# Kernel optimization log

Measured on AMD Instinct MI355X. Metric: run time of the kernel, lower is better.

## Reference

```python
import jax, jax.numpy as jnp
import numpy as np

B, Q, K = 16, 100, 100
H, DM = 8, 512
DK = DM // H          # 64, per-head dim (= Attention embed_dim)
MID = 32              # mid_dim
EPS = 1e-5            # GroupNorm eps
NEG = -1000000000.0   # masked_fill value


def setup_inputs() -> dict:
    key = jax.random.key(0)
    ks = jax.random.split(key, 32)
    def n(k, shape, s=0.02):
        return jax.random.normal(k, shape, jnp.float32) * s
    inp = {
        "query": jax.random.normal(ks[0], (B, Q, DM), jnp.float32),
        "key":   jax.random.normal(ks[1], (B, K, DM), jnp.float32),
        "value": jax.random.normal(ks[2], (B, K, DM), jnp.float32),
        "mask":  jnp.ones((B, Q, K), jnp.float32),
        # 4 input projections: Linear(DM,DM) -> CELU -> GroupNorm(H, DM)
        "Wq1": n(ks[3], (DM, DM)), "bq1": jnp.zeros((DM,), jnp.float32),
        "gw1": jnp.ones((DM,), jnp.float32), "gb1": jnp.zeros((DM,), jnp.float32),
        "Wk":  n(ks[4], (DM, DM)), "bk":  jnp.zeros((DM,), jnp.float32),
        "gwk": jnp.ones((DM,), jnp.float32), "gbk": jnp.zeros((DM,), jnp.float32),
        "Wq2": n(ks[5], (DM, DM)), "bq2": jnp.zeros((DM,), jnp.float32),
        "gw2": jnp.ones((DM,), jnp.float32), "gb2": jnp.zeros((DM,), jnp.float32),
        "Wv":  n(ks[6], (DM, DM)), "bv":  jnp.zeros((DM,), jnp.float32),
        "gwv": jnp.ones((DM,), jnp.float32), "gbv": jnp.zeros((DM,), jnp.float32),
        # Attention MLPs (per-head, embed_dim = DK)
        "We":  n(ks[7], (MID, DK)), "be":  jnp.zeros((MID,), jnp.float32),
        "Ws":  n(ks[8], (1, MID)),  "bs":  jnp.zeros((1,), jnp.float32),
        "Wsq": n(ks[9], (DK, MID)), "bsq": jnp.zeros((DK,), jnp.float32),
    }
    return inp


def _proj(x, W, b, gw, gb):
    """Linear -> CELU -> GroupNorm(H groups over DM channels), then split heads.
    x: (B, L, DM) -> (B, H, L, DK)"""
    Bn, L, _ = x.shape
    y = jax.nn.celu(x.reshape(Bn * L, DM) @ W.T + b)
    yg = y.reshape(Bn * L, H, DK)
    mu = yg.mean(-1, keepdims=True)
    var = yg.var(-1, keepdims=True)
    yn = ((yg - mu) * jax.lax.rsqrt(var + EPS)).reshape(Bn * L, DM)
    yn = yn * gw + gb
    return yn.reshape(Bn, L, H, DK).transpose(0, 2, 1, 3)


def reference(query, key, value, mask,
              Wq1, bq1, gw1, gb1, Wk, bk, gwk, gbk,
              Wq2, bq2, gw2, gb2, Wv, bv, gwv, gbv,
              We, be, Ws, bs, Wsq, bsq):
    q1 = _proj(query, Wq1, bq1, gw1, gb1)   # (B,H,Q,DK)
    k  = _proj(key,   Wk,  bk,  gwk, gbk)   # (B,H,K,DK)
    q2 = _proj(query, Wq2, bq2, gw2, gb2)   # (B,H,Q,DK)
    v  = _proj(value, Wv,  bv,  gwv, gbv)   # (B,H,K,DK)

    m = mask[:, None]                        # (B,1,Q,K)
    # bilinear query-key map, embedded by Linear->ReLU (dropout=identity, eval)
    key_map = jnp.einsum('bhqd,bhkd->bhqkd', q1, k)          # (B,H,Q,K,DK)
    km = jax.nn.relu(jnp.einsum('bhqkd,md->bhqkm', key_map, We) + be)  # (B,H,Q,K,MID)

    alpha = jnp.einsum('bhqkm,m->bhqk', km, Ws[0]) + bs[0]   # (B,H,Q,K)
    alpha = jnp.where(m == 0, NEG, alpha)
    alpha = jax.nn.softmax(alpha, axis=-1)

    # masked mean pooling over K, then channel squeeze-excite
    pool = jnp.sum(km * m[..., None], axis=-2) / jnp.sum(m[..., None], axis=-2)  # (B,H,Q,MID)
    ch = jax.nn.sigmoid(pool @ Wsq.T + bsq)                  # (B,H,Q,DK)

    # spatial attention over val_map: sum_k alpha * (q2_d * v_kd) = q2 * (alpha @ v)
    sp = q2 * jnp.einsum('bhqk,bhkd->bhqd', alpha, v)        # (B,H,Q,DK)
    x = sp * ch
    return x.transpose(0, 2, 1, 3).reshape(x.shape[0], -1, DM)  # (B,Q,DM)
```

## Files before the change

kernel.cpp:

```cpp
#include <hip/hip_runtime.h>
#include <hip/hip_bf16.h>
#include <math.h>

#define H 8
#define DM 512
#define DK 64
#define MID 32
#define LL 100
#define EPS 1e-5f
#define NEGV -1000000000.0f

typedef unsigned short u16;
typedef __attribute__((ext_vector_type(8))) short short8b;
typedef __attribute__((ext_vector_type(16))) float f32x16;

#define MFMA32 __builtin_amdgcn_mfma_f32_32x32x16_bf16
#define GLD_LDS16(g, l) __builtin_amdgcn_global_load_lds( \
    (const __attribute__((address_space(1))) void*)(g), \
    (__attribute__((address_space(3))) void*)(l), 16, 0, 0)

__device__ __forceinline__ unsigned pkbf2(float a, float b) {
    union { __hip_bfloat162 h; unsigned u; } cv;
    cv.h = __float22bfloat162_rn(make_float2(a, b));
    return cv.u;
}
__device__ __forceinline__ u16 bfbits(float a) {
    union { __hip_bfloat16 b; u16 u; } cv;
    cv.b = __float2bfloat16(a);
    return cv.u;
}
__device__ __forceinline__ float bf2f(u16 u) {
    union { u16 u; __hip_bfloat16 b; } cv; cv.u = u;
    return __bfloat162float(cv.b);
}

__global__ __launch_bounds__(256) void cvt_kernel(
    const float* __restrict__ q, const float* __restrict__ k, const float* __restrict__ v,
    const float* __restrict__ w1, const float* __restrict__ wk,
    const float* __restrict__ w2, const float* __restrict__ wv,
    u16* __restrict__ qh, u16* __restrict__ qlo, u16* __restrict__ kh, u16* __restrict__ klo,
    u16* __restrict__ vh, u16* __restrict__ vlo,
    u16* __restrict__ w1h, u16* __restrict__ w1l, u16* __restrict__ wkh, u16* __restrict__ wkl,
    u16* __restrict__ w2h, u16* __restrict__ w2l, u16* __restrict__ wvh, u16* __restrict__ wvl)
{
    int f = blockIdx.x * 256 + threadIdx.x;
    const float* src; u16* dh; u16* dl; int off;
    if (f < 204800)      { src = q;  dh = qh;  dl = qlo; off = f; }
    else if (f < 409600) { src = k;  dh = kh;  dl = klo; off = f - 204800; }
    else if (f < 614400) { src = v;  dh = vh;  dl = vlo; off = f - 409600; }
    else if (f < 679936) { src = w1; dh = w1h; dl = w1l; off = f - 614400; }
    else if (f < 745472) { src = wk; dh = wkh; dl = wkl; off = f - 679936; }
    else if (f < 811008) { src = w2; dh = w2h; dl = w2l; off = f - 745472; }
    else                 { src = wv; dh = wvh; dl = wvl; off = f - 811008; }
    float4 x = *(const float4*)(src + (size_t)off * 4);
    u16 h0 = bfbits(x.x), h1 = bfbits(x.y), h2 = bfbits(x.z), h3 = bfbits(x.w);
    ushort4 hv; hv.x = h0; hv.y = h1; hv.z = h2; hv.w = h3;
    ushort4 lv;
    lv.x = bfbits(x.x - bf2f(h0)); lv.y = bfbits(x.y - bf2f(h1));
    lv.z = bfbits(x.z - bf2f(h2)); lv.w = bfbits(x.w - bf2f(h3));
    *(ushort4*)(dh + (size_t)off * 4) = hv;
    *(ushort4*)(dl + (size_t)off * 4) = lv;
}

__global__ __launch_bounds__(256) void proj_kernel(
    const u16* __restrict__ qh, const u16* __restrict__ qlo,
    const u16* __restrict__ kh, const u16* __restrict__ klo,
    const u16* __restrict__ vh, const u16* __restrict__ vlo,
    const u16* __restrict__ w1h, const u16* __restrict__ w1l,
    const u16* __restrict__ wkh, const u16* __restrict__ wkl,
    const u16* __restrict__ w2h, const u16* __restrict__ w2l,
    const u16* __restrict__ wvh, const u16* __restrict__ wvl,
    const float* __restrict__ bq1, const float* __restrict__ gw1, const float* __restrict__ gb1,
    const float* __restrict__ bk , const float* __restrict__ gwk, const float* __restrict__ gbk,
    const float* __restrict__ bq2, const float* __restrict__ gw2, const float* __restrict__ gb2,
    const float* __restrict__ bv , const float* __restrict__ gwv, const float* __restrict__ gbv,
    float* __restrict__ q1o, u16* __restrict__ kbf,
    float* __restrict__ q2o, u16* __restrict__ vtbf)
{
    __shared__ u16 sm[20480];
    __shared__ float lds_s[4][32];
    __shared__ float lds_q[4][32];
    u16* Xh = sm;          u16* Xl = sm + 2048;
    u16* Wh = sm + 4096;   u16* Wl = sm + 12288;

    const int rt = blockIdx.x;
    const int ct = blockIdx.y;
    const int p  = blockIdx.z;
    const int j0 = ct * 128;
    const int r0 = rt * 32;
    const int t = threadIdx.x, w = t >> 6, lane = t & 63, ql = lane & 31, hf = lane >> 5;

    const u16 *Xhg, *Xlg, *Whg, *Wlg; const float *bias, *gw, *gb;
    if (p == 0)      { Xhg=qh; Xlg=qlo; Whg=w1h; Wlg=w1l; bias=bq1; gw=gw1; gb=gb1; }
    else if (p == 1) { Xhg=kh; Xlg=klo; Whg=wkh; Wlg=wkl; bias=bk;  gw=gwk; gb=gbk; }
    else if (p == 2) { Xhg=qh; Xlg=qlo; Whg=w2h; Wlg=w2l; bias=bq2; gw=gw2; gb=gb2; }
    else             { Xhg=vh; Xlg=vlo; Whg=wvh; Wlg=wvl; bias=bv;  gw=gwv; gb=gbv; }

    f32x16 acc = {0.f,0.f,0.f,0.f,0.f,0.f,0.f,0.f,0.f,0.f,0.f,0.f,0.f,0.f,0.f,0.f};

    for (int kc = 0; kc < 8; ++kc) {
        __syncthreads();
        for (int i = w; i < 40; i += 4) {
            const u16* g; u16* l; int blk, rbase;
            if (i < 4)       { g = Xhg; l = Xh; blk = i;      rbase = r0; }
            else if (i < 8)  { g = Xlg; l = Xl; blk = i - 4;  rbase = r0; }
            else if (i < 24) { g = Whg; l = Wh; blk = i - 8;  rbase = j0; }
            else             { g = Wlg; l = Wl; blk = i - 24; rbase = j0; }
            int row = blk * 8 + (lane >> 3);
            int k16 = (lane & 7) ^ (row & 7);
            const u16* ga = g + (size_t)(rbase + row) * 512 + kc * 64 + k16 * 8;
            GLD_LDS16(ga, (char*)l + blk * 1024);
        }
        __syncthreads();
        const int brow = w * 32 + ql;
        #pragma unroll
        for (int ks = 0; ks < 4; ++ks) {
            int slot = (ks * 2 + hf) ^ (ql & 7);
            short8b Ah = *(const short8b*)(Xh + ql * 64 + slot * 8);
            short8b Al = *(const short8b*)(Xl + ql * 64 + slot * 8);
            short8b Bh = *(const short8b*)(Wh + brow * 64 + slot * 8);
            short8b Bl = *(const short8b*)(Wl + brow * 64 + slot * 8);
            acc = MFMA32(Ah, Bh, acc, 0, 0, 0);
            acc = MFMA32(Ah, Bl, acc, 0, 0, 0);
            acc = MFMA32(Al, Bh, acc, 0, 0, 0);
        }
    }

    const int colg = j0 + w * 32 + ql;
    const float bv_ = bias[colg];
    const float gwc = gw[colg], gbc = gb[colg];
    float y[16], s[16], sq[16];
    #pragma unroll
    for (int r = 0; r < 16; ++r) {
        float x = acc[r] + bv_;
        x = x > 0.f ? x : expm1f(x);
        y[r] = x; s[r] = x; sq[r] = x * x;
    }
    #pragma unroll
    for (int off = 1; off < 32; off <<= 1) {
        #pragma unroll
        for (int r = 0; r < 16; ++r) {
            s[r]  += __shfl_xor(s[r],  off, 64);
            sq[r] += __shfl_xor(sq[r], off, 64);
        }
    }
    if (ql == 0) {
        #pragma unroll
        for (int r = 0; r < 16; ++r) {
            int row = (r & 3) + 8 * (r >> 2) + 4 * hf;
            lds_s[w][row] = s[r]; lds_q[w][row] = sq[r];
        }
    }
    __syncthreads();
    const int wp = w ^ 1;
    const int hh = colg >> 6, dk = colg & 63;
    #pragma unroll
    for (int r = 0; r < 16; ++r) {
        int row = (r & 3) + 8 * (r >> 2) + 4 * hf;
        float sum = lds_s[w][row] + lds_s[wp][row];
        float ssq = lds_q[w][row] + lds_q[wp][row];
        float mu  = sum * (1.f / 64.f);
        float var = ssq * (1.f / 64.f) - mu * mu;
        float inv = rsqrtf(var + EPS);
        float yn  = (y[r] - mu) * inv * gwc + gbc;
        int rg = r0 + row;
        int b = rg / 100;
        int l = rg - b * 100;
        size_t bh = (size_t)(b * H + hh);
        if (p == 0)      q1o[(bh * 100 + l) * 64 + dk] = yn;
        else if (p == 2) q2o[(bh * 100 + l) * 64 + dk] = yn;
        else if (p == 1) kbf[(bh * 128 + l) * 64 + dk] = bfbits(yn);
        else             vtbf[(bh * 64 + dk) * 128 + l] = bfbits(yn);
    }
}

__global__ __launch_bounds__(256, 2) void attn_kernel(
    const float* __restrict__ q1o, const u16* __restrict__ kbf,
    const float* __restrict__ q2o, const u16* __restrict__ vtbf,
    const float* __restrict__ mask,
    const float* __restrict__ We, const float* __restrict__ be,
    const float* __restrict__ Wsv, const float* __restrict__ bs,
    const float* __restrict__ Wsq, const float* __restrict__ bsq,
    float* __restrict__ out)
{
    __shared__ float lds_We[32 * 64];
    __shared__ float lds_score[128 * 33];
    __shared__ float lds_pool[2][32 * 33];
    __shared__ float lds_of[2][16 * 64];
    __shared__ float lds_mx[2][32], lds_se[2][32], lds_ms[2][32];

    const int bh = blockIdx.x, b = bh >> 3, h = bh & 7, qt = blockIdx.y;
    const int tid = threadIdx.x;
    const int w = tid >> 6, lane = tid & 63;
    const int wk = w >> 1, wm = w & 1;
    const int ql = lane & 31, hf = lane >> 5;
    const int q0 = qt * 32, q = q0 + ql;
    const int qc = q < 100 ? q : 99;

    for (int i = tid * 4; i < 2048; i += 1024)
        *(float4*)(lds_We + i) = *(const float4*)(We + i);
    for (int i = tid; i < 2 * 32 * 33; i += 256)
        ((float*)lds_pool)[i] = 0.f;

    const u16* kb = kbf + (size_t)bh * 128 * 64;
    short8b A[2][4];
    #pragma unroll
    for (int mtl = 0; mtl < 2; ++mtl)
        #pragma unroll
        for (int ks = 0; ks < 4; ++ks)
            A[mtl][ks] = *(const short8b*)(kb + (size_t)((2 * wk + mtl) * 32 + ql) * 64 + ks * 16 + hf * 8);

    float q1r[4][8];
    const float* q1p = q1o + ((size_t)bh * 100 + qc) * 64;
    #pragma unroll
    for (int ks = 0; ks < 4; ++ks) {
        float4 u0 = *(const float4*)(q1p + ks * 16 + hf * 8);
        float4 u1 = *(const float4*)(q1p + ks * 16 + hf * 8 + 4);
        q1r[ks][0] = u0.x; q1r[ks][1] = u0.y; q1r[ks][2] = u0.z; q1r[ks][3] = u0.w;
        q1r[ks][4] = u1.x; q1r[ks][5] = u1.y; q1r[ks][6] = u1.z; q1r[ks][7] = u1.w;
    }
    const float bsv = bs[0];

    float sc[2][16];
    #pragma unroll
    for (int mtl = 0; mtl < 2; ++mtl)
        #pragma unroll
        for (int r = 0; r < 16; ++r) sc[mtl][r] = 0.f;

    __syncthreads();

    for (int mi = 0; mi < 16; ++mi) {
        const int m = wm * 16 + mi;
        const float bem = be[m], wsm = Wsv[m];
        short8b Bf[4];
        #pragma unroll
        for (int ks = 0; ks < 4; ++ks) {
            const float* wp_ = lds_We + m * 64 + ks * 16 + hf * 8;
            float4 w0 = *(const float4*)(wp_);
            float4 w1 = *(const float4*)(wp_ + 4);
            union { unsigned u[4]; short8b v; } pk;
            pk.u[0] = pkbf2(w0.x * q1r[ks][0], w0.y * q1r[ks][1]);
            pk.u[1] = pkbf2(w0.z * q1r[ks][2], w0.w * q1r[ks][3]);
            pk.u[2] = pkbf2(w1.x * q1r[ks][4], w1.y * q1r[ks][5]);
            pk.u[3] = pkbf2(w1.z * q1r[ks][6], w1.w * q1r[ks][7]);
            Bf[ks] = pk.v;
        }
        #pragma unroll
        for (int mtl = 0; mtl < 2; ++mtl) {
            const int mt = 2 * wk + mtl;
            f32x16 c = {0.f,0.f,0.f,0.f,0.f,0.f,0.f,0.f,0.f,0.f,0.f,0.f,0.f,0.f,0.f,0.f};
            c = MFMA32(A[mtl][0], Bf[0], c, 0, 0, 0);
            c = MFMA32(A[mtl][1], Bf[1], c, 0, 0, 0);
            c = MFMA32(A[mtl][2], Bf[2], c, 0, 0, 0);
            c = MFMA32(A[mtl][3], Bf[3], c, 0, 0, 0);
            float psum = 0.f, psum4 = 0.f;
            #pragma unroll
            for (int r = 0; r < 16; ++r) {
                float tv = fmaxf(c[r] + bem, 0.f);
                sc[mtl][r] = fmaf(tv, wsm, sc[mtl][r]);
                if (mt != 3) psum += tv;
                else if (r < 4) psum4 += tv;
            }
            if (mt == 3) psum = (hf == 0) ? psum4 : 0.f;
            psum += __shfl_xor(psum, 32, 64);
            if (hf == 0) lds_pool[wk][ql * 33 + m] += psum;
        }
    }

    float msum = 0.f;
    const float* mrow = mask + ((size_t)b * 100 + qc) * 100;
    #pragma unroll
    for (int mtl = 0; mtl < 2; ++mtl) {
        const int mt = 2 * wk + mtl;
        #pragma unroll
        for (int g = 0; g < 4; ++g) {
            int k0 = mt * 32 + g * 8 + hf * 4;
            if (k0 < 100) {
                float4 mk = *(const float4*)(mrow + k0);
                msum += mk.x + mk.y + mk.z + mk.w;
                if (mk.x == 0.f) sc[mtl][g * 4 + 0] = NEGV;
                if (mk.y == 0.f) sc[mtl][g * 4 + 1] = NEGV;
                if (mk.z == 0.f) sc[mtl][g * 4 + 2] = NEGV;
                if (mk.w == 0.f) sc[mtl][g * 4 + 3] = NEGV;
            } else {
                sc[mtl][g * 4 + 0] = -INFINITY; sc[mtl][g * 4 + 1] = -INFINITY;
                sc[mtl][g * 4 + 2] = -INFINITY; sc[mtl][g * 4 + 3] = -INFINITY;
            }
        }
    }
    msum += __shfl_xor(msum, 32, 64);

    if (wm == 0) {
        #pragma unroll
        for (int mtl = 0; mtl < 2; ++mtl)
            #pragma unroll
            for (int r = 0; r < 16; ++r) {
                int row = (2 * wk + mtl) * 32 + (r & 3) + 8 * (r >> 2) + 4 * hf;
                lds_score[row * 33 + ql] = sc[mtl][r];
            }
    }
    __syncthreads();
    if (wm == 1) {
        #pragma unroll
        for (int mtl = 0; mtl < 2; ++mtl)
            #pragma unroll
            for (int r = 0; r < 16; ++r) {
                int row = (2 * wk + mtl) * 32 + (r & 3) + 8 * (r >> 2) + 4 * hf;
                lds_score[row * 33 + ql] += sc[mtl][r];
            }
    }
    __syncthreads();

    float mx = -INFINITY;
    #pragma unroll
    for (int mtl = 0; mtl < 2; ++mtl)
        #pragma unroll
        for (int r = 0; r < 16; ++r) {
            int row = (2 * wk + mtl) * 32 + (r & 3) + 8 * (r >> 2) + 4 * hf;
            float sv = lds_score[row * 33 + ql] + bsv;
            sc[mtl][r] = sv;
            mx = fmaxf(mx, sv);
        }
    mx = fmaxf(mx, __shfl_xor(mx, 32, 64));
    if (hf == 0 && wm == 0) { lds_mx[wk][ql] = mx; lds_ms[wk][ql] = msum; }
    __syncthreads();
    mx = fmaxf(lds_mx[0][ql], lds_mx[1][ql]);
    const float msumT = lds_ms[0][ql] + lds_ms[1][ql];
    float se = 0.f;
    #pragma unroll
    for (int mtl = 0; mtl < 2; ++mtl)
        #pragma unroll
        for (int r = 0; r < 16; ++r) {
            float ev = expf(sc[mtl][r] - mx);
            sc[mtl][r] = ev;
            se += ev;
        }
    se += __shfl_xor(se, 32, 64);
    if (hf == 0 && wm == 0) lds_se[wk][ql] = se;
    __syncthreads();
    const float inv_se = 1.f / (lds_se[0][ql] + lds_se[1][ql]);
    #pragma unroll
    for (int mtl = 0; mtl < 2; ++mtl)
        #pragma unroll
        for (int r = 0; r < 16; ++r) sc[mtl][r] *= inv_se;

    const int nks = 4 - wk;
    short8b A2[4];
    #pragma unroll
    for (int ksl = 0; ksl < 4; ++ksl) {
        if (ksl < nks) {
            const int s_ = ksl & 1, mtl = ksl >> 1;
            unsigned a0 = pkbf2(sc[mtl][8 * s_ + 0], sc[mtl][8 * s_ + 1]);
            unsigned a1 = pkbf2(sc[mtl][8 * s_ + 2], sc[mtl][8 * s_ + 3]);
            unsigned b0 = pkbf2(sc[mtl][8 * s_ + 4], sc[mtl][8 * s_ + 5]);
            unsigned b1 = pkbf2(sc[mtl][8 * s_ + 6], sc[mtl][8 * s_ + 7]);
            unsigned o0 = hf ? b0 : a0, o1 = hf ? b1 : a1;
            unsigned s0 = hf ? a0 : b0, s1 = hf ? a1 : b1;
            unsigned r0_ = (unsigned)__shfl_xor((int)s0, 32, 64);
            unsigned r1_ = (unsigned)__shfl_xor((int)s1, 32, 64);
            union { unsigned u[4]; short8b v; } pk;
            pk.u[0] = hf ? r0_ : o0;  pk.u[1] = hf ? r1_ : o1;
            pk.u[2] = hf ? o0 : r0_;  pk.u[3] = hf ? o1 : r1_;
            A2[ksl] = pk.v;
        }
    }

    const u16* vb = vtbf + (size_t)bh * 64 * 128 + (size_t)(wm * 32 + ql) * 128;
    f32x16 o = {0.f,0.f,0.f,0.f,0.f,0.f,0.f,0.f,0.f,0.f,0.f,0.f,0.f,0.f,0.f,0.f};
    #pragma unroll
    for (int ksl = 0; ksl < 4; ++ksl) {
        if (ksl < nks) {
            short8b vf = *(const short8b*)(vb + (4 * wk + ksl) * 16 + hf * 8);
            o = MFMA32(A2[ksl], vf, o, 0, 0, 0);
        }
    }

    if (wk == 0) {
        #pragma unroll
        for (int r = 0; r < 16; ++r) lds_of[wm][r * 64 + lane] = o[r];
    }
    __syncthreads();
    if (wk == 1) {
        #pragma unroll
        for (int r = 0; r < 16; ++r) o[r] += lds_of[wm][r * 64 + lane];

        const float invm = 1.f / msumT;
        short8b A3[2], B3[2];
        #pragma unroll
        for (int ks = 0; ks < 2; ++ks) {
            const float* p0_ = lds_pool[0] + ql * 33 + ks * 16 + hf * 8;
            const float* p1_ = lds_pool[1] + ql * 33 + ks * 16 + hf * 8;
            union { unsigned u[4]; short8b v; } pk;
            pk.u[0] = pkbf2((p0_[0]+p1_[0])*invm, (p0_[1]+p1_[1])*invm);
            pk.u[1] = pkbf2((p0_[2]+p1_[2])*invm, (p0_[3]+p1_[3])*invm);
            pk.u[2] = pkbf2((p0_[4]+p1_[4])*invm, (p0_[5]+p1_[5])*invm);
            pk.u[3] = pkbf2((p0_[6]+p1_[6])*invm, (p0_[7]+p1_[7])*invm);
            A3[ks] = pk.v;
            const float* wqp = Wsq + (size_t)(wm * 32 + ql) * 32 + ks * 16 + hf * 8;
            float4 c0 = *(const float4*)(wqp);
            float4 c1 = *(const float4*)(wqp + 4);
            union { unsigned u[4]; short8b v; } pk2;
            pk2.u[0] = pkbf2(c0.x, c0.y); pk2.u[1] = pkbf2(c0.z, c0.w);
            pk2.u[2] = pkbf2(c1.x, c1.y); pk2.u[3] = pkbf2(c1.z, c1.w);
            B3[ks] = pk2.v;
        }
        f32x16 z = {0.f,0.f,0.f,0.f,0.f,0.f,0.f,0.f,0.f,0.f,0.f,0.f,0.f,0.f,0.f,0.f};
        z = MFMA32(A3[0], B3[0], z, 0, 0, 0);
        z = MFMA32(A3[1], B3[1], z, 0, 0, 0);

        const float bsqv = bsq[wm * 32 + ql];
        const float* q2p = q2o + (size_t)bh * 100 * 64;
        const int dcol = wm * 32 + ql;
        #pragma unroll
        for (int r = 0; r < 16; ++r) {
            int qr = q0 + (r & 3) + 8 * (r >> 2) + 4 * hf;
            if (qr < 100) {
                float chv = 1.f / (1.f + expf(-(z[r] + bsqv)));
                float ov  = o[r] * chv * q2p[(size_t)qr * 64 + dcol];
                out[((size_t)(b * 100 + qr)) * DM + h * 64 + dcol] = ov;
            }
        }
    }
}

extern "C" void kernel_launch(void* const* d_in, const int* in_sizes, int n_in,
                              void* d_out, int out_size, void* d_ws, size_t ws_size,
                              hipStream_t stream)
{
    const float* query = (const float*)d_in[0];
    const float* key   = (const float*)d_in[1];
    const float* value = (const float*)d_in[2];
    const float* mask  = (const float*)d_in[3];
    const float* Wq1 = (const float*)d_in[4];
    const float* bq1 = (const float*)d_in[5];
    const float* gw1 = (const float*)d_in[6];
    const float* gb1 = (const float*)d_in[7];
    const float* Wk  = (const float*)d_in[8];
    const float* bk  = (const float*)d_in[9];
    const float* gwk = (const float*)d_in[10];
    const float* gbk = (const float*)d_in[11];
    const float* Wq2 = (const float*)d_in[12];
    const float* bq2 = (const float*)d_in[13];
    const float* gw2 = (const float*)d_in[14];
    const float* gb2 = (const float*)d_in[15];
    const float* Wv  = (const float*)d_in[16];
    const float* bv  = (const float*)d_in[17];
    const float* gwv = (const float*)d_in[18];
    const float* gbv = (const float*)d_in[19];
    const float* We  = (const float*)d_in[20];
    const float* be  = (const float*)d_in[21];
    const float* Ws  = (const float*)d_in[22];
    const float* bs  = (const float*)d_in[23];
    const float* Wsq = (const float*)d_in[24];
    const float* bsq = (const float*)d_in[25];

    float* wsf = (float*)d_ws;
    float* q1o = wsf;
    float* q2o = wsf + 819200;
    u16* kbf   = (u16*)(wsf + 1638400);
    u16* vtbf  = kbf + 1048576;
    u16* c0    = vtbf + 1048576;
    u16 *qh = c0, *qlo = qh + 819200, *khh = qlo + 819200, *klo = khh + 819200,
        *vhh = klo + 819200, *vlo = vhh + 819200;
    u16* wbase = vlo + 819200;
    u16 *w1h = wbase,          *w1l = w1h + 262144,
        *wkh = w1l + 262144,   *wkl = wkh + 262144,
        *w2h = wkl + 262144,   *w2l = w2h + 262144,
        *wvh = w2l + 262144,   *wvl = wvh + 262144;

    cvt_kernel<<<3424, 256, 0, stream>>>(query, key, value, Wq1, Wk, Wq2, Wv,
        qh, qlo, khh, klo, vhh, vlo, w1h, w1l, wkh, wkl, w2h, w2l, wvh, wvl);

    dim3 g1(50, 4, 4);
    proj_kernel<<<g1, 256, 0, stream>>>(
        qh, qlo, khh, klo, vhh, vlo, w1h, w1l, wkh, wkl, w2h, w2l, wvh, wvl,
        bq1, gw1, gb1, bk, gwk, gbk, bq2, gw2, gb2, bv, gwv, gbv,
        q1o, kbf, q2o, vtbf);

    dim3 g2(128, 4);
    attn_kernel<<<g2, 256, 0, stream>>>(q1o, kbf, q2o, vtbf, mask,
        We, be, Ws, bs, Wsq, bsq, (float*)d_out);
}
```

Before: 193.1 us.

## Pre-swizzle bf16 split operands into MFMA fragment layout and drop LDS staging

```diff
diff --git a/kernel.cpp b/kernel.cpp
--- a/kernel.cpp
+++ b/kernel.cpp
@@ -15,9 +15,6 @@
 typedef __attribute__((ext_vector_type(16))) float f32x16;
 
 #define MFMA32 __builtin_amdgcn_mfma_f32_32x32x16_bf16
-#define GLD_LDS16(g, l) __builtin_amdgcn_global_load_lds( \
-    (const __attribute__((address_space(1))) void*)(g), \
-    (__attribute__((address_space(3))) void*)(l), 16, 0, 0)
 
 __device__ __forceinline__ unsigned pkbf2(float a, float b) {
     union { __hip_bfloat162 h; unsigned u; } cv;
@@ -43,23 +40,41 @@
     u16* __restrict__ w1h, u16* __restrict__ w1l, u16* __restrict__ wkh, u16* __restrict__ wkl,
     u16* __restrict__ w2h, u16* __restrict__ w2l, u16* __restrict__ wvh, u16* __restrict__ wvl)
 {
-    int f = blockIdx.x * 256 + threadIdx.x;
-    const float* src; u16* dh; u16* dl; int off;
-    if (f < 204800)      { src = q;  dh = qh;  dl = qlo; off = f; }
-    else if (f < 409600) { src = k;  dh = kh;  dl = klo; off = f - 204800; }
-    else if (f < 614400) { src = v;  dh = vh;  dl = vlo; off = f - 409600; }
-    else if (f < 679936) { src = w1; dh = w1h; dl = w1l; off = f - 614400; }
-    else if (f < 745472) { src = wk; dh = wkh; dl = wkl; off = f - 679936; }
-    else if (f < 811008) { src = w2; dh = w2h; dl = w2l; off = f - 745472; }
-    else                 { src = wv; dh = wvh; dl = wvl; off = f - 811008; }
-    float4 x = *(const float4*)(src + (size_t)off * 4);
-    u16 h0 = bfbits(x.x), h1 = bfbits(x.y), h2 = bfbits(x.z), h3 = bfbits(x.w);
-    ushort4 hv; hv.x = h0; hv.y = h1; hv.z = h2; hv.w = h3;
-    ushort4 lv;
-    lv.x = bfbits(x.x - bf2f(h0)); lv.y = bfbits(x.y - bf2f(h1));
-    lv.z = bfbits(x.z - bf2f(h2)); lv.w = bfbits(x.w - bf2f(h3));
-    *(ushort4*)(dh + (size_t)off * 4) = hv;
-    *(ushort4*)(dl + (size_t)off * 4) = lv;
+    int g = blockIdx.x * 256 + threadIdx.x;
+    const float* src; u16 *dh, *dl; int off;
+    if (g < 307200) {
+        int a = g / 102400;
+        off = g - a * 102400;
+        src = a == 0 ? q : (a == 1 ? k : v);
+        dh  = a == 0 ? qh : (a == 1 ? kh : vh);
+        dl  = a == 0 ? qlo : (a == 1 ? klo : vlo);
+    } else {
+        int gg = g - 307200;
+        int a = gg >> 15;
+        off = gg & 32767;
+        src = a == 0 ? w1 : (a == 1 ? wk : (a == 2 ? w2 : wv));
+        dh  = a == 0 ? w1h : (a == 1 ? wkh : (a == 2 ? w2h : wvh));
+        dl  = a == 0 ? w1l : (a == 1 ? wkl : (a == 2 ? w2l : wvl));
+    }
+    const int rr = off & 31, hf = (off >> 5) & 1, kb = (off >> 6) & 31, tile = off >> 11;
+    const float* sp = src + ((size_t)(tile * 32 + rr)) * 512 + kb * 16 + hf * 8;
+    float4 x0 = *(const float4*)sp;
+    float4 x1 = *(const float4*)(sp + 4);
+    float xs[8] = {x0.x, x0.y, x0.z, x0.w, x1.x, x1.y, x1.z, x1.w};
+    u16 hb[8], lb[8];
+    #pragma unroll
+    for (int j = 0; j < 8; ++j) {
+        hb[j] = bfbits(xs[j]);
+        lb[j] = bfbits(xs[j] - bf2f(hb[j]));
+    }
+    ushort4 h0; h0.x = hb[0]; h0.y = hb[1]; h0.z = hb[2]; h0.w = hb[3];
+    ushort4 h1; h1.x = hb[4]; h1.y = hb[5]; h1.z = hb[6]; h1.w = hb[7];
+    ushort4 l0; l0.x = lb[0]; l0.y = lb[1]; l0.z = lb[2]; l0.w = lb[3];
+    ushort4 l1; l1.x = lb[4]; l1.y = lb[5]; l1.z = lb[6]; l1.w = lb[7];
+    *(ushort4*)(dh + (size_t)off * 8)     = h0;
+    *(ushort4*)(dh + (size_t)off * 8 + 4) = h1;
+    *(ushort4*)(dl + (size_t)off * 8)     = l0;
+    *(ushort4*)(dl + (size_t)off * 8 + 4) = l1;
 }
 
 __global__ __launch_bounds__(256) void proj_kernel(
@@ -77,18 +92,14 @@
     float* __restrict__ q1o, u16* __restrict__ kbf,
     float* __restrict__ q2o, u16* __restrict__ vtbf)
 {
-    __shared__ u16 sm[20480];
     __shared__ float lds_s[4][32];
     __shared__ float lds_q[4][32];
-    u16* Xh = sm;          u16* Xl = sm + 2048;
-    u16* Wh = sm + 4096;   u16* Wl = sm + 12288;
 
     const int rt = blockIdx.x;
     const int ct = blockIdx.y;
     const int p  = blockIdx.z;
-    const int j0 = ct * 128;
-    const int r0 = rt * 32;
     const int t = threadIdx.x, w = t >> 6, lane = t & 63, ql = lane & 31, hf = lane >> 5;
+    const int wr = w >> 1, wc = w & 1;
 
     const u16 *Xhg, *Xlg, *Whg, *Wlg; const float *bias, *gw, *gb;
     if (p == 0)      { Xhg=qh; Xlg=qlo; Whg=w1h; Wlg=w1l; bias=bq1; gw=gw1; gb=gb1; }
@@ -96,37 +107,26 @@
     else if (p == 2) { Xhg=qh; Xlg=qlo; Whg=w2h; Wlg=w2l; bias=bq2; gw=gw2; gb=gb2; }
     else             { Xhg=vh; Xlg=vlo; Whg=wvh; Wlg=wvl; bias=bv;  gw=gwv; gb=gbv; }
 
+    const int rtile = rt * 2 + wr;
+    const int ctile = ct * 2 + wc;
+    const u16* pAh = Xhg + (size_t)rtile * 16384 + hf * 256 + ql * 8;
+    const u16* pAl = Xlg + (size_t)rtile * 16384 + hf * 256 + ql * 8;
+    const u16* pBh = Whg + (size_t)ctile * 16384 + hf * 256 + ql * 8;
+    const u16* pBl = Wlg + (size_t)ctile * 16384 + hf * 256 + ql * 8;
+
     f32x16 acc = {0.f,0.f,0.f,0.f,0.f,0.f,0.f,0.f,0.f,0.f,0.f,0.f,0.f,0.f,0.f,0.f};
-
-    for (int kc = 0; kc < 8; ++kc) {
-        __syncthreads();
-        for (int i = w; i < 40; i += 4) {
-            const u16* g; u16* l; int blk, rbase;
-            if (i < 4)       { g = Xhg; l = Xh; blk = i;      rbase = r0; }
-            else if (i < 8)  { g = Xlg; l = Xl; blk = i - 4;  rbase = r0; }
-            else if (i < 24) { g = Whg; l = Wh; blk = i - 8;  rbase = j0; }
-            else             { g = Wlg; l = Wl; blk = i - 24; rbase = j0; }
-            int row = blk * 8 + (lane >> 3);
-            int k16 = (lane & 7) ^ (row & 7);
-            const u16* ga = g + (size_t)(rbase + row) * 512 + kc * 64 + k16 * 8;
-            GLD_LDS16(ga, (char*)l + blk * 1024);
-        }
-        __syncthreads();
-        const int brow = w * 32 + ql;
-        #pragma unroll
-        for (int ks = 0; ks < 4; ++ks) {
-            int slot = (ks * 2 + hf) ^ (ql & 7);
-            short8b Ah = *(const short8b*)(Xh + ql * 64 + slot * 8);
-            short8b Al = *(const short8b*)(Xl + ql * 64 + slot * 8);
-            short8b Bh = *(const short8b*)(Wh + brow * 64 + slot * 8);
-            short8b Bl = *(const short8b*)(Wl + brow * 64 + slot * 8);
-            acc = MFMA32(Ah, Bh, acc, 0, 0, 0);
-            acc = MFMA32(Ah, Bl, acc, 0, 0, 0);
-            acc = MFMA32(Al, Bh, acc, 0, 0, 0);
-        }
-    }
-
-    const int colg = j0 + w * 32 + ql;
+    #pragma unroll 4
+    for (int kb = 0; kb < 32; ++kb) {
+        short8b Ah = *(const short8b*)(pAh + kb * 512);
+        short8b Al = *(const short8b*)(pAl + kb * 512);
+        short8b Bh = *(const short8b*)(pBh + kb * 512);
+        short8b Bl = *(const short8b*)(pBl + kb * 512);
+        acc = MFMA32(Ah, Bh, acc, 0, 0, 0);
+        acc = MFMA32(Ah, Bl, acc, 0, 0, 0);
+        acc = MFMA32(Al, Bh, acc, 0, 0, 0);
+    }
+
+    const int colg = ct * 64 + wc * 32 + ql;
     const float bv_ = bias[colg];
     const float gwc = gw[colg], gbc = gb[colg];
     float y[16], s[16], sq[16];
@@ -153,7 +153,8 @@
     }
     __syncthreads();
     const int wp = w ^ 1;
-    const int hh = colg >> 6, dk = colg & 63;
+    const int hh = ct, dk = wc * 32 + ql;
+    const int r0 = rt * 64 + wr * 32;
     #pragma unroll
     for (int r = 0; r < 16; ++r) {
         int row = (r & 3) + 8 * (r >> 2) + 4 * hf;
@@ -468,10 +469,10 @@
         *w2h = wkl + 262144,   *w2l = w2h + 262144,
         *wvh = w2l + 262144,   *wvl = wvh + 262144;
 
-    cvt_kernel<<<3424, 256, 0, stream>>>(query, key, value, Wq1, Wk, Wq2, Wv,
+    cvt_kernel<<<1712, 256, 0, stream>>>(query, key, value, Wq1, Wk, Wq2, Wv,
         qh, qlo, khh, klo, vhh, vlo, w1h, w1l, wkh, wkl, w2h, w2l, wvh, wvl);
 
-    dim3 g1(50, 4, 4);
+    dim3 g1(25, 8, 4);
     proj_kernel<<<g1, 256, 0, stream>>>(
         qh, qlo, khh, klo, vhh, vlo, w1h, w1l, wkh, wkl, w2h, w2l, wvh, wvl,
         bq1, gw1, gb1, bk, gwk, gbk, bq2, gw2, gb2, bv, gwv, gbv,
```

Measured after the change: 182.2 us. 1.06x faster.
